# Optimization experiments

Measured on AMD Instinct MI355X. Metric: run time of the kernel, lower is better.

Reference implementation:

```python
import jax, jax.numpy as jnp
import numpy as np

EPS_BN = 1e-5
EPS_LN = 1e-5

def _bn(x, gamma, beta, ch_axis):
    # training-mode BatchNorm: batch stats over all axes except ch_axis (biased var)
    axes = tuple(i for i in range(x.ndim) if i != ch_axis)
    mean = x.mean(axes, keepdims=True)
    var = x.var(axes, keepdims=True)
    shp = [1] * x.ndim; shp[ch_axis] = -1
    return (x - mean) / jnp.sqrt(var + EPS_BN) * gamma.reshape(shp) + beta.reshape(shp)

def _ln(x, gamma, beta):
    mean = x.mean(-1, keepdims=True)
    var = x.var(-1, keepdims=True)
    return (x - mean) / jnp.sqrt(var + EPS_LN) * gamma + beta

def _spline(x, knots, cps):
    # x: (B,S); knots, cps: (K,). Single-pass bucketize + gather + lerp,
    # equivalent to the torch per-interval masked loop (boundary points take
    # the right interval's t=0 value, identical result).
    K = knots.shape[0]
    xn = (x - jnp.min(x)) / (jnp.max(x) - jnp.min(x) + 1e-6)
    idx = jnp.clip(jnp.searchsorted(knots, xn, side='right') - 1, 0, K - 2)
    k0, k1 = knots[idx], knots[idx + 1]
    t = (xn - k0) / (k1 - k0)
    val = (1.0 - t) * cps[idx] + t * cps[idx + 1]
    in_range = (xn >= knots[0]) & (xn <= knots[-1])
    return jnp.where(in_range, val, 0.0)

def _mha(x, in_w, in_b, out_w, out_b, H):
    # torch nn.MultiheadAttention with batch_first=False: dim0 is the sequence.
    L, N, D = x.shape
    hd = D // H
    qkv = x @ in_w.T + in_b                       # (L,N,3D)
    q, k, v = jnp.split(qkv, 3, axis=-1)
    q = q.reshape(L, N, H, hd) * (1.0 / np.sqrt(hd))
    k = k.reshape(L, N, H, hd)
    v = v.reshape(L, N, H, hd)
    scores = jnp.einsum('lnhd,mnhd->nhlm', q, k)  # (N,H,L,L)
    attn = jax.nn.softmax(scores, axis=-1)
    out = jnp.einsum('nhlm,mnhd->lnhd', attn, v).reshape(L, N, D)
    return out @ out_w.T + out_b

def setup_inputs() -> dict:
    B, S, D, F, K, H = 32, 1024, 512, 8, 32, 8
    key = jax.random.key(0)
    ks = jax.random.split(key, 12)
    s = 0.02
    inp = {
        'x': jax.random.normal(ks[0], (B, S, D), jnp.float32),
        'in_w': jax.random.normal(ks[1], (3 * D, D), jnp.float32) * s,
        'in_b': jnp.zeros((3 * D,), jnp.float32),
        'out_w': jax.random.normal(ks[2], (D, D), jnp.float32) * s,
        'out_b': jnp.zeros((D,), jnp.float32),
        'attn_g': jnp.ones((D,), jnp.float32),
        'attn_beta': jnp.zeros((D,), jnp.float32),
        'proj_w': jax.random.normal(ks[3], (F, D), jnp.float32) * s,
        'proj_b': jnp.zeros((F,), jnp.float32),
        'pn_g': jnp.ones((F,), jnp.float32),
        'pn_beta': jnp.zeros((F,), jnp.float32),
        'knots': jnp.tile(jnp.linspace(0.0, 1.0, K, dtype=jnp.float32)[None, :], (F, 1)),
        'cps': jax.random.normal(ks[4], (F, K), jnp.float32) / np.sqrt(K),
        'gate_w': jax.random.normal(ks[5], (2 * D, F), jnp.float32) * s,
        'gate_b': jnp.zeros((2 * D,), jnp.float32),
        'gbn_g': jnp.ones((S,), jnp.float32),   # BatchNorm1d(2*d_model) hits dim1 = seq (= 2*d_model)
        'gbn_beta': jnp.zeros((S,), jnp.float32),
        'ln_g': jnp.ones((D,), jnp.float32),
        'ln_beta': jnp.zeros((D,), jnp.float32),
        'outp_w': jax.random.normal(ks[6], (D, D), jnp.float32) * s,
        'outp_b': jnp.zeros((D,), jnp.float32),
        'on_g': jnp.ones((D,), jnp.float32),
        'on_beta': jnp.zeros((D,), jnp.float32),
    }
    return inp

def reference(x, in_w, in_b, out_w, out_b, attn_g, attn_beta, proj_w, proj_b,
              pn_g, pn_beta, knots, cps, gate_w, gate_b, gbn_g, gbn_beta,
              ln_g, ln_beta, outp_w, outp_b, on_g, on_beta):
    H = 8
    attn_out = _mha(x, in_w, in_b, out_w, out_b, H)          # (B,S,D)
    attn_out = _bn(attn_out, attn_g, attn_beta, 2)
    projected = x @ proj_w.T + proj_b                         # (B,S,F)
    projected = _bn(projected, pn_g, pn_beta, 2)
    transformed = jax.vmap(_spline, in_axes=(2, 0, 0), out_axes=2)(projected, knots, cps)  # (B,S,F)
    h = transformed @ gate_w.T + gate_b                       # (B,S,2D)
    h = _bn(h, gbn_g, gbn_beta, 1)                            # channel axis = seq (torch quirk)
    a, b = jnp.split(h, 2, axis=-1)
    glu = a * jax.nn.sigmoid(b)                               # (B,S,D)
    gated = _ln(glu, ln_g, ln_beta)
    out = gated @ outp_w.T + outp_b
    out = _bn(out, on_g, on_beta, 2)
    return x + attn_out + out
```

## Files before the change

### kernel.cpp

```cpp
#include <hip/hip_runtime.h>
#include <math.h>


#define SOFF_AMEAN 0
#define SOFF_ARSTD 512
#define SOFF_OMEAN 1024
#define SOFF_ORSTD 1536
#define SOFF_PMEAN 2048
#define SOFF_PRSTD 2056
#define SOFF_FMIN  2064
#define SOFF_FMAX  2072
#define SOFF_SMEAN 2080
#define SOFF_SRSTD 3104
#define SOFF_G1    4128
#define SOFF_GB    4136
#define SOFF_SGB   4144
#define SOFF_QGB   4145
#define SOFF_G2    4160
#define SOFF_PART  4224

typedef short bf16x8_t __attribute__((ext_vector_type(8)));
typedef float f32x4_t __attribute__((ext_vector_type(4)));
typedef unsigned short us8_t __attribute__((ext_vector_type(8)));

__device__ __forceinline__ unsigned short f2bf(float f) {
  unsigned u = __float_as_uint(f);
  u = (u + 0x7FFFu + ((u >> 16) & 1u)) >> 16;
  return (unsigned short)u;
}
__device__ __forceinline__ float b2f(unsigned short u) {
  return __uint_as_float(((unsigned)u) << 16);
}

#define BARR do { asm volatile("" ::: "memory"); __builtin_amdgcn_s_barrier(); asm volatile("" ::: "memory"); } while (0)

__global__ __launch_bounds__(256) void zero_kernel(float* __restrict__ p) {
  p[blockIdx.x * 256 + threadIdx.x] = 0.f;
}

__global__ __launch_bounds__(256) void cvt8_kernel(const float* __restrict__ src,
                                                   unsigned short* __restrict__ dst) {
  int i = blockIdx.x * 256 + threadIdx.x;
  float4 a = ((const float4*)src)[i * 2];
  float4 b = ((const float4*)src)[i * 2 + 1];
  us8_t o;
  o[0] = f2bf(a.x); o[1] = f2bf(a.y); o[2] = f2bf(a.z); o[3] = f2bf(a.w);
  o[4] = f2bf(b.x); o[5] = f2bf(b.y); o[6] = f2bf(b.z); o[7] = f2bf(b.w);
  *(us8_t*)(dst + (size_t)i * 8) = o;
}

template<int NT, bool OUT_BF16, bool STATS>
__global__ __launch_bounds__(512, 2) void gemm256_kernel(
    const unsigned short* __restrict__ A, const unsigned short* __restrict__ B,
    const float* __restrict__ bias, unsigned short* __restrict__ Cb,
    float* __restrict__ Cf, float* __restrict__ gstats, int N) {
  __shared__ unsigned short As[2][256 * 64];
  __shared__ unsigned short Bs[2][256 * 64];
  const int bi = blockIdx.x;
  const int xcd = bi & 7, jb = bi >> 3;
  const int m0 = (xcd * 16 + jb / NT) * 256;
  const int n0 = (jb % NT) * 256;
  const int t = threadIdx.x;
  const int w = t >> 6, lane = t & 63;
  const int wm = w >> 2, wn = w & 3;

  const int srow = lane >> 3;
  const int sgo = ((lane & 7) ^ srow) * 8;
  const unsigned short* gA = A + (size_t)(m0 + w * 32 + srow) * 512 + sgo;
  const unsigned short* gB = B + (size_t)(n0 + w * 32 + srow) * 512 + sgo;

  const int fr = lane & 15, g = lane >> 4;
  const int swz = fr & 7;

  f32x4_t acc[8][4];
#pragma unroll
  for (int i = 0; i < 8; ++i)
#pragma unroll
    for (int jj = 0; jj < 4; ++jj) acc[i][jj] = (f32x4_t){0.f, 0.f, 0.f, 0.f};

#define STAGE(SX, KO) do { \
  _Pragma("unroll") for (int jj = 0; jj < 4; ++jj) { \
    __builtin_amdgcn_global_load_lds( \
        (const __attribute__((address_space(1))) void*)(gA + (size_t)jj * 8 * 512 + (KO)), \
        (__attribute__((address_space(3))) void*)&As[SX][(w * 32 + jj * 8) * 64], 16, 0, 0); \
    __builtin_amdgcn_global_load_lds( \
        (const __attribute__((address_space(1))) void*)(gB + (size_t)jj * 8 * 512 + (KO)), \
        (__attribute__((address_space(3))) void*)&Bs[SX][(w * 32 + jj * 8) * 64], 16, 0, 0); \
  } \
} while (0)

#define RDA(MI0) do { \
  _Pragma("unroll") for (int m2 = 0; m2 < 2; ++m2) \
    _Pragma("unroll") for (int ks = 0; ks < 2; ++ks) \
      af[m2][ks] = *(const bf16x8_t*)&as[((wm * 128 + (MI0 + m2) * 16 + fr) * 64) + (((ks * 4 + g) ^ swz) * 8)]; \
} while (0)

#define QUAD(MI0) do { \
  __builtin_amdgcn_s_setprio(1); \
  _Pragma("unroll") for (int ks = 0; ks < 2; ++ks) \
    _Pragma("unroll") for (int m2 = 0; m2 < 2; ++m2) \
      _Pragma("unroll") for (int ni = 0; ni < 4; ++ni) \
        acc[MI0 + m2][ni] = __builtin_amdgcn_mfma_f32_16x16x32_bf16(af[m2][ks], bfr[ni][ks], acc[MI0 + m2][ni], 0, 0, 0); \
  __builtin_amdgcn_s_setprio(0); \
} while (0)

  STAGE(0, (size_t)0);
  asm volatile("s_waitcnt vmcnt(0)" ::: "memory");
  BARR;

#pragma unroll 2
  for (int kt = 0; kt < 8; ++kt) {
    const int sd = kt & 1;
    const unsigned short* as = &As[sd][0];
    const unsigned short* bs = &Bs[sd][0];
    bf16x8_t bfr[4][2], af[2][2];

#pragma unroll
    for (int ni = 0; ni < 4; ++ni)
#pragma unroll
      for (int ks = 0; ks < 2; ++ks)
        bfr[ni][ks] = *(const bf16x8_t*)&bs[((wn * 64 + ni * 16 + fr) * 64) + (((ks * 4 + g) ^ swz) * 8)];
    RDA(0);
    if (kt < 7) STAGE(sd ^ 1, (size_t)(kt + 1) * 64);
    BARR;
    QUAD(0);
    BARR;
    RDA(2);
    BARR;
    QUAD(2);
    BARR;
    RDA(4);
    BARR;
    QUAD(4);
    BARR;
    RDA(6);
    BARR;
    QUAD(6);
    if (kt < 7) asm volatile("s_waitcnt vmcnt(0)" ::: "memory");
    BARR;
  }

  const int cr = (lane >> 4) * 4, cc = lane & 15;
#pragma unroll
  for (int ni = 0; ni < 4; ++ni) {
    int col = n0 + wn * 64 + ni * 16 + cc;
    float bv = bias[col];
    float lsum = 0.f, lsq = 0.f;
#pragma unroll
    for (int mi = 0; mi < 8; ++mi) {
#pragma unroll
      for (int jj = 0; jj < 4; ++jj) {
        int row = m0 + wm * 128 + mi * 16 + cr + jj;
        float v = acc[mi][ni][jj] + bv;
        if (OUT_BF16) Cb[(size_t)row * N + col] = f2bf(v);
        else          Cf[(size_t)row * N + col] = v;
        if (STATS) { lsum += v; lsq += v * v; }
      }
    }
    if (STATS) {
      lsum += __shfl_xor(lsum, 16); lsum += __shfl_xor(lsum, 32);
      lsq  += __shfl_xor(lsq, 16);  lsq  += __shfl_xor(lsq, 32);
      if (lane < 16) {
        atomicAdd(&gstats[col], lsum);
        atomicAdd(&gstats[512 + col], lsq);
      }
    }
  }
#undef STAGE
#undef RDA
#undef QUAD
}

__global__ __launch_bounds__(512) void statsfin_kernel(const float* __restrict__ part,
                                                       float* __restrict__ stats, int off) {
  int t = threadIdx.x;
  float mean = part[t] / 32768.f;
  float var = part[512 + t] / 32768.f - mean * mean;
  stats[off + t] = mean;
  stats[off + 512 + t] = rsqrtf(var + 1e-5f);
}

__global__ __launch_bounds__(256) void attn2_kernel(const unsigned short* __restrict__ qkv,
                                                    unsigned short* __restrict__ ctxb) {
  const int n = blockIdx.x, h = blockIdx.y, t = threadIdx.x;
  __shared__ float qs[32 * 68], ks[32 * 68], vs[32 * 68], ss[32 * 33];
  const int l = t >> 3, j0 = (t & 7) * 8;
  size_t rowb = ((size_t)(l * 1024 + n)) * 1536 + h * 64 + j0;
  us8_t qv = *(const us8_t*)(qkv + rowb);
  us8_t kv = *(const us8_t*)(qkv + rowb + 512);
  us8_t vv = *(const us8_t*)(qkv + rowb + 1024);
#pragma unroll
  for (int j = 0; j < 8; ++j) {
    qs[l * 68 + j0 + j] = b2f(qv[j]) * 0.125f;
    ks[l * 68 + j0 + j] = b2f(kv[j]);
    vs[l * 68 + j0 + j] = b2f(vv[j]);
  }
  __syncthreads();
  for (int o = t; o < 1024; o += 256) {
    int ll = o >> 5, m = o & 31;
    const float4* q4 = (const float4*)&qs[ll * 68];
    const float4* k4 = (const float4*)&ks[m * 68];
    float s = 0.f;
#pragma unroll
    for (int dd = 0; dd < 16; ++dd) {
      float4 a = q4[dd], b = k4[dd];
      s += a.x * b.x + a.y * b.y + a.z * b.z + a.w * b.w;
    }
    ss[ll * 33 + m] = s;
  }
  __syncthreads();
  if (t < 32) {
    float mx = -3e38f;
    for (int m = 0; m < 32; ++m) mx = fmaxf(mx, ss[t * 33 + m]);
    float sum = 0.f;
    for (int m = 0; m < 32; ++m) { float e = __expf(ss[t * 33 + m] - mx); ss[t * 33 + m] = e; sum += e; }
    float inv = 1.f / sum;
    for (int m = 0; m < 32; ++m) ss[t * 33 + m] *= inv;
  }
  __syncthreads();
  float o[8] = {0.f, 0.f, 0.f, 0.f, 0.f, 0.f, 0.f, 0.f};
#pragma unroll 8
  for (int m = 0; m < 32; ++m) {
    float pm = ss[l * 33 + m];
    const float* vr = &vs[m * 68 + j0];
#pragma unroll
    for (int j = 0; j < 8; ++j) o[j] += pm * vr[j];
  }
  us8_t ov;
#pragma unroll
  for (int j = 0; j < 8; ++j) ov[j] = f2bf(o[j]);
  *(us8_t*)(ctxb + ((size_t)(l * 1024 + n)) * 512 + h * 64 + j0) = ov;
}

__global__ __launch_bounds__(256) void proj_kernel(const float* __restrict__ x,
    const float* __restrict__ pw, const float* __restrict__ pb, float* __restrict__ p) {
  int blk = blockIdx.x, t = threadIdx.x;
  int r0 = blk * 64;
  __shared__ float xsp[64 * 33];
  __shared__ float pwc[8 * 33];
  int l = t >> 2, fg = t & 3;
  float acc0 = 0.f, acc1 = 0.f;
  for (int k0 = 0; k0 < 512; k0 += 32) {
    __syncthreads();
    for (int i = t; i < 2048; i += 256) { int ll = i >> 5, kk = i & 31; xsp[ll * 33 + kk] = x[(size_t)(r0 + ll) * 512 + k0 + kk]; }
    { int ff = t >> 5, kk = t & 31; pwc[ff * 33 + kk] = pw[ff * 512 + k0 + kk]; }
    __syncthreads();
#pragma unroll 8
    for (int kk = 0; kk < 32; ++kk) {
      float xv = xsp[l * 33 + kk];
      acc0 += xv * pwc[(fg * 2) * 33 + kk];
      acc1 += xv * pwc[(fg * 2 + 1) * 33 + kk];
    }
  }
  float2 o; o.x = acc0 + pb[fg * 2]; o.y = acc1 + pb[fg * 2 + 1];
  *(float2*)&p[(r0 + l) * 8 + fg * 2] = o;
}

__global__ __launch_bounds__(256) void projstats_kernel(const float* __restrict__ p,
                                                        float* __restrict__ part) {
  int t = threadIdx.x, blk = blockIdx.x;
  int f = t & 7;
  float s = 0.f, s2 = 0.f;
  for (int r = blk * 32 + (t >> 3); r < 32768; r += 2048) { float v = p[r * 8 + f]; s += v; s2 += v * v; }
  __shared__ float red[256], red2[256];
  red[t] = s; red2[t] = s2; __syncthreads();
  for (int off = 128; off >= 8; off >>= 1) { if (t < off) { red[t] += red[t + off]; red2[t] += red2[t + off]; } __syncthreads(); }
  if (t < 8) { part[blk * 16 + t] = red[t]; part[blk * 16 + 8 + t] = red2[t]; }
}
__global__ void projfin_kernel(const float* __restrict__ part, float* __restrict__ stats) {
  int t = threadIdx.x;
  if (t < 8) {
    float s = 0.f, s2 = 0.f;
    for (int b = 0; b < 64; ++b) { s += part[b * 16 + t]; s2 += part[b * 16 + 8 + t]; }
    float mean = s / 32768.f;
    float var = s2 / 32768.f - mean * mean;
    stats[SOFF_PMEAN + t] = mean;
    stats[SOFF_PRSTD + t] = rsqrtf(var + 1e-5f);
  }
}

__global__ __launch_bounds__(256) void bnminmax_kernel(float* __restrict__ p,
    const float* __restrict__ stats, const float* __restrict__ png,
    const float* __restrict__ pnb, float* __restrict__ part) {
  int t = threadIdx.x, blk = blockIdx.x;
  int i0 = blk * 256 + t;
  int f = i0 & 7;
  float k1 = stats[SOFF_PRSTD + f] * png[f];
  float k0 = pnb[f] - stats[SOFF_PMEAN + f] * k1;
  float mn = 3e38f, mx = -3e38f;
  for (int i = i0; i < 262144; i += 16384) {
    float v = p[i] * k1 + k0;
    p[i] = v;
    mn = fminf(mn, v); mx = fmaxf(mx, v);
  }
  __shared__ float rmn[256], rmx[256];
  rmn[t] = mn; rmx[t] = mx; __syncthreads();
  for (int off = 128; off >= 8; off >>= 1) {
    if (t < off) { rmn[t] = fminf(rmn[t], rmn[t + off]); rmx[t] = fmaxf(rmx[t], rmx[t + off]); }
    __syncthreads();
  }
  if (t < 8) { part[blk * 16 + t] = rmn[t]; part[blk * 16 + 8 + t] = rmx[t]; }
}
__global__ void minmaxfin_kernel(const float* __restrict__ part, float* __restrict__ stats) {
  int t = threadIdx.x;
  if (t < 8) {
    float mn = 3e38f, mx = -3e38f;
    for (int b = 0; b < 64; ++b) { mn = fminf(mn, part[b * 16 + t]); mx = fmaxf(mx, part[b * 16 + 8 + t]); }
    stats[SOFF_FMIN + t] = mn;
    stats[SOFF_FMAX + t] = mx;
  }
}

__global__ __launch_bounds__(256) void spline_kernel(float* __restrict__ p,
    const float* __restrict__ knots, const float* __restrict__ cps,
    const float* __restrict__ stats) {
  __shared__ float ksh[8 * 33], csh[8 * 33];
  int t = threadIdx.x;
  { int f = t >> 5, j = t & 31; ksh[f * 33 + j] = knots[t]; csh[f * 33 + j] = cps[t]; }
  __syncthreads();
  int i = blockIdx.x * 256 + t;
  int f = i & 7;
  float xv = p[i];
  float mn = stats[SOFF_FMIN + f], mx = stats[SOFF_FMAX + f];
  float xn = (xv - mn) / (mx - mn + 1e-6f);
  const float* kn = &ksh[f * 33];
  const float* cp = &csh[f * 33];
  int pcnt = 0;
#pragma unroll
  for (int j = 0; j < 32; ++j) pcnt += (kn[j] <= xn) ? 1 : 0;
  int idx = pcnt - 1;
  idx = idx < 0 ? 0 : (idx > 30 ? 30 : idx);
  float k0v = kn[idx], k1v = kn[idx + 1];
  float tt = (xn - k0v) / (k1v - k0v);
  float val = (1.f - tt) * cp[idx] + tt * cp[idx + 1];
  bool inr = (xn >= kn[0]) && (xn <= kn[31]);
  p[i] = inr ? val : 0.f;
}

__global__ __launch_bounds__(256) void gateprep_kernel(const float* __restrict__ gw,
    const float* __restrict__ gb, float* __restrict__ stats) {
  int b = blockIdx.x, t = threadIdx.x;
  __shared__ float red[256];
  float s = 0.f;
  if (b < 64) {
    int f1 = b >> 3, f2 = b & 7;
    for (int j = t; j < 1024; j += 256) s += gw[j * 8 + f1] * gw[j * 8 + f2];
  } else if (b < 72) {
    int f = b - 64;
    for (int j = t; j < 1024; j += 256) s += gw[j * 8 + f];
  } else if (b < 80) {
    int f = b - 72;
    for (int j = t; j < 1024; j += 256) s += gb[j] * gw[j * 8 + f];
  } else if (b == 80) {
    for (int j = t; j < 1024; j += 256) s += gb[j];
  } else {
    for (int j = t; j < 1024; j += 256) s += gb[j] * gb[j];
  }
  red[t] = s; __syncthreads();
  for (int off = 128; off > 0; off >>= 1) { if (t < off) red[t] += red[t + off]; __syncthreads(); }
  if (t == 0) {
    float v = red[0];
    if (b < 64) stats[SOFF_G2 + b] = v;
    else if (b < 72) stats[SOFF_G1 + (b - 64)] = v;
    else if (b < 80) stats[SOFF_GB + (b - 72)] = v;
    else if (b == 80) stats[SOFF_SGB] = v;
    else stats[SOFF_QGB] = v;
  }
}

__global__ __launch_bounds__(256) void sstats_kernel(const float* __restrict__ tbuf,
                                                     float* __restrict__ stats) {
  int s = blockIdx.x, t = threadIdx.x;
  __shared__ float tv[256];
  __shared__ float red[256];
  __shared__ float T1[8];
  __shared__ float Ms[64];
  int b = t >> 3, f = t & 7;
  tv[t] = tbuf[(b * 1024 + s) * 8 + f];
  __syncthreads();
  red[t] = tv[t]; __syncthreads();
  for (int off = 128; off >= 8; off >>= 1) { if (t < off) red[t] += red[t + off]; __syncthreads(); }
  if (t < 8) T1[t] = red[t];
  if (t < 64) {
    int f1 = t >> 3, f2 = t & 7; float sM = 0.f;
    for (int bb = 0; bb < 32; ++bb) sM += tv[bb * 8 + f1] * tv[bb * 8 + f2];
    Ms[t] = sM;
  }
  __syncthreads();
  if (t == 0) {
    float sh = 0.f, s2 = 0.f;
    for (int ff = 0; ff < 8; ++ff) {
      sh += stats[SOFF_G1 + ff] * T1[ff];
      s2 += 2.f * stats[SOFF_GB + ff] * T1[ff];
    }
    sh += 32.f * stats[SOFF_SGB];
    for (int i = 0; i < 64; ++i) s2 += Ms[i] * stats[SOFF_G2 + i];
    s2 += 32.f * stats[SOFF_QGB];
    float mean = sh / 32768.f;
    float var = s2 / 32768.f - mean * mean;
    stats[SOFF_SMEAN + s] = mean;
    stats[SOFF_SRSTD + s] = rsqrtf(var + 1e-5f);
  }
}

__global__ __launch_bounds__(256) void gluln_kernel(const float* __restrict__ tbuf,
    const float* __restrict__ gw, const float* __restrict__ gb,
    const float* __restrict__ stats, const float* __restrict__ gbng,
    const float* __restrict__ gbnb, const float* __restrict__ lng,
    const float* __restrict__ lnb, unsigned short* __restrict__ gatedb) {
  const int t = threadIdx.x, wave = t >> 6, lane = t & 63;
  for (int rr = 0; rr < 4; ++rr) {
    const int r = blockIdx.x * 16 + wave * 4 + rr;
    const int s = r & 1023;
    float4 tA = *(const float4*)&tbuf[r * 8];
    float4 tB = *(const float4*)&tbuf[r * 8 + 4];
    float smean = stats[SOFF_SMEAN + s], srstd = stats[SOFF_SRSTD + s];
    float k1 = srstd * gbng[s];
    float k0 = gbnb[s] - smean * k1;
    float g[8];
    float sum = 0.f, sq = 0.f;
#pragma unroll
    for (int i = 0; i < 8; ++i) {
      int c = i * 64 + lane;
      float4 wa0 = *(const float4*)&gw[c * 8];
      float4 wa1 = *(const float4*)&gw[c * 8 + 4];
      float4 wb0 = *(const float4*)&gw[(c + 512) * 8];
      float4 wb1 = *(const float4*)&gw[(c + 512) * 8 + 4];
      float ha = tA.x * wa0.x + tA.y * wa0.y + tA.z * wa0.z + tA.w * wa0.w
               + tB.x * wa1.x + tB.y * wa1.y + tB.z * wa1.z + tB.w * wa1.w + gb[c];
      float hb = tA.x * wb0.x + tA.y * wb0.y + tA.z * wb0.z + tA.w * wb0.w
               + tB.x * wb1.x + tB.y * wb1.y + tB.z * wb1.z + tB.w * wb1.w + gb[c + 512];
      ha = ha * k1 + k0;
      hb = hb * k1 + k0;
      float gv = ha / (1.f + __expf(-hb));
      g[i] = gv; sum += gv; sq += gv * gv;
    }
#pragma unroll
    for (int m = 32; m >= 1; m >>= 1) { sum += __shfl_xor(sum, m); sq += __shfl_xor(sq, m); }
    float mean = sum * (1.f / 512.f);
    float rstd = rsqrtf(sq * (1.f / 512.f) - mean * mean + 1e-5f);
#pragma unroll
    for (int i = 0; i < 8; ++i) {
      int c = i * 64 + lane;
      gatedb[(size_t)r * 512 + c] = f2bf((g[i] - mean) * rstd * lng[c] + lnb[c]);
    }
  }
}

__global__ __launch_bounds__(256) void final_kernel(const float* __restrict__ x,
    const float* __restrict__ attn, const float* __restrict__ outl,
    const float* __restrict__ stats, const float* __restrict__ ag,
    const float* __restrict__ ab, const float* __restrict__ og,
    const float* __restrict__ ob, float* __restrict__ y) {
  int idx = blockIdx.x * 256 + threadIdx.x;
  int c4 = (idx & 127) * 4;
  float4 xv = ((const float4*)x)[idx];
  float4 av = ((const float4*)attn)[idx];
  float4 ov = ((const float4*)outl)[idx];
  float4 am = *(const float4*)&stats[SOFF_AMEAN + c4];
  float4 ar = *(const float4*)&stats[SOFF_ARSTD + c4];
  float4 om = *(const float4*)&stats[SOFF_OMEAN + c4];
  float4 orr = *(const float4*)&stats[SOFF_ORSTD + c4];
  float4 g1 = *(const float4*)&ag[c4];
  float4 b1 = *(const float4*)&ab[c4];
  float4 g2 = *(const float4*)&og[c4];
  float4 b2 = *(const float4*)&ob[c4];
  float4 o;
  o.x = xv.x + (av.x - am.x) * ar.x * g1.x + b1.x + (ov.x - om.x) * orr.x * g2.x + b2.x;
  o.y = xv.y + (av.y - am.y) * ar.y * g1.y + b1.y + (ov.y - om.y) * orr.y * g2.y + b2.y;
  o.z = xv.z + (av.z - am.z) * ar.z * g1.z + b1.z + (ov.z - om.z) * orr.z * g2.z + b2.z;
  o.w = xv.w + (av.w - am.w) * ar.w * g1.w + b1.w + (ov.w - om.w) * orr.w * g2.w + b2.w;
  ((float4*)y)[idx] = o;
}

extern "C" void kernel_launch(void* const* d_in, const int* in_sizes, int n_in,
                              void* d_out, int out_size, void* d_ws, size_t ws_size,
                              hipStream_t stream) {
  (void)in_sizes; (void)n_in; (void)out_size; (void)ws_size;
  const float* x        = (const float*)d_in[0];
  const float* in_w     = (const float*)d_in[1];
  const float* in_b     = (const float*)d_in[2];
  const float* out_w    = (const float*)d_in[3];
  const float* out_b    = (const float*)d_in[4];
  const float* attn_g   = (const float*)d_in[5];
  const float* attn_bt  = (const float*)d_in[6];
  const float* proj_w   = (const float*)d_in[7];
  const float* proj_b   = (const float*)d_in[8];
  const float* pn_g     = (const float*)d_in[9];
  const float* pn_bt    = (const float*)d_in[10];
  const float* knots    = (const float*)d_in[11];
  const float* cps      = (const float*)d_in[12];
  const float* gate_w   = (const float*)d_in[13];
  const float* gate_b   = (const float*)d_in[14];
  const float* gbn_g    = (const float*)d_in[15];
  const float* gbn_bt   = (const float*)d_in[16];
  const float* ln_g     = (const float*)d_in[17];
  const float* ln_bt    = (const float*)d_in[18];
  const float* outp_w   = (const float*)d_in[19];
  const float* outp_b   = (const float*)d_in[20];
  const float* on_g     = (const float*)d_in[21];
  const float* on_bt    = (const float*)d_in[22];

  float* out = (float*)d_out;
  unsigned short* xb      = (unsigned short*)d_ws;
  unsigned short* qkv_b   = xb + 16777216;
  unsigned short* ctx_b   = qkv_b + 50331648;
  unsigned short* wqkv_b  = ctx_b + 16777216;
  unsigned short* wout_b  = wqkv_b + 786432;
  unsigned short* woutp_b = wout_b + 262144;
  float* proj  = (float*)(woutp_b + 262144);
  float* stats = proj + 262144;
  float* part  = stats + SOFF_PART;
  float* partA  = part;
  float* partO  = part + 1024;
  float* partP  = part + 2048;
  float* partMM = part + 3072;
  float* attnf = (float*)qkv_b;
  unsigned short* gated_b = xb;

  zero_kernel<<<dim3(8), dim3(256), 0, stream>>>(part);
  cvt8_kernel<<<dim3(8192), dim3(256), 0, stream>>>(x, xb);
  cvt8_kernel<<<dim3(384), dim3(256), 0, stream>>>(in_w, wqkv_b);
  cvt8_kernel<<<dim3(128), dim3(256), 0, stream>>>(out_w, wout_b);
  cvt8_kernel<<<dim3(128), dim3(256), 0, stream>>>(outp_w, woutp_b);
  gemm256_kernel<6, true, false><<<dim3(768), dim3(512), 0, stream>>>(
      xb, wqkv_b, in_b, qkv_b, nullptr, nullptr, 1536);
  attn2_kernel<<<dim3(1024, 8), dim3(256), 0, stream>>>(qkv_b, ctx_b);
  gemm256_kernel<2, false, true><<<dim3(256), dim3(512), 0, stream>>>(
      ctx_b, wout_b, out_b, nullptr, attnf, partA, 512);
  statsfin_kernel<<<dim3(1), dim3(512), 0, stream>>>(partA, stats, SOFF_AMEAN);
  proj_kernel<<<dim3(512), dim3(256), 0, stream>>>(x, proj_w, proj_b, proj);
  projstats_kernel<<<dim3(64), dim3(256), 0, stream>>>(proj, partP);
  projfin_kernel<<<dim3(1), dim3(64), 0, stream>>>(partP, stats);
  bnminmax_kernel<<<dim3(64), dim3(256), 0, stream>>>(proj, stats, pn_g, pn_bt, partMM);
  minmaxfin_kernel<<<dim3(1), dim3(64), 0, stream>>>(partMM, stats);
  spline_kernel<<<dim3(1024), dim3(256), 0, stream>>>(proj, knots, cps, stats);
  gateprep_kernel<<<dim3(88), dim3(256), 0, stream>>>(gate_w, gate_b, stats);
  sstats_kernel<<<dim3(1024), dim3(256), 0, stream>>>(proj, stats);
  gluln_kernel<<<dim3(2048), dim3(256), 0, stream>>>(proj, gate_w, gate_b, stats,
                                                     gbn_g, gbn_bt, ln_g, ln_bt, gated_b);
  gemm256_kernel<2, false, true><<<dim3(256), dim3(512), 0, stream>>>(
      gated_b, woutp_b, outp_b, nullptr, out, partO, 512);
  statsfin_kernel<<<dim3(1), dim3(512), 0, stream>>>(partO, stats, SOFF_OMEAN);
  final_kernel<<<dim3(16384), dim3(256), 0, stream>>>(x, attnf, out, stats,
                                                      attn_g, attn_bt, on_g, on_bt, out);
}
```

Before: 534.0 us.

## Restructure GEMM main loop into 4-stage K=32 LDS pipeline with single barrier

The 256x256 bf16 GEMM now streams K in 32-wide slices through a 4-deep LDS ring (prefetch distance 3) instead of 64-wide double buffering. Each iteration loads all A/B fragments and issues 32 MFMAs with one barrier, instead of four read/compute phases separated by many barriers. The epilogue is also reordered to iterate rows outer and columns inner, with per-column partial stats. The aim is to hide global load latency and cut barrier overhead. In exchange it keeps more fragment registers live and uses a new LDS swizzle for the narrower rows.

```diff
diff --git a/kernel.cpp b/kernel.cpp
--- a/kernel.cpp
+++ b/kernel.cpp
@@ -54,8 +54,8 @@
     const unsigned short* __restrict__ A, const unsigned short* __restrict__ B,
     const float* __restrict__ bias, unsigned short* __restrict__ Cb,
     float* __restrict__ Cf, float* __restrict__ gstats, int N) {
-  __shared__ unsigned short As[2][256 * 64];
-  __shared__ unsigned short Bs[2][256 * 64];
+  __shared__ unsigned short As[4][256 * 32];
+  __shared__ unsigned short Bs[4][256 * 32];
   const int bi = blockIdx.x;
   const int xcd = bi & 7, jb = bi >> 3;
   const int m0 = (xcd * 16 + jb / NT) * 256;
@@ -64,13 +64,13 @@
   const int w = t >> 6, lane = t & 63;
   const int wm = w >> 2, wn = w & 3;
 
-  const int srow = lane >> 3;
-  const int sgo = ((lane & 7) ^ srow) * 8;
-  const unsigned short* gA = A + (size_t)(m0 + w * 32 + srow) * 512 + sgo;
-  const unsigned short* gB = B + (size_t)(n0 + w * 32 + srow) * 512 + sgo;
+  const unsigned short* gA = A + (size_t)(m0 + w * 16 + (lane >> 2)) * 512
+                               + (((lane & 3) ^ ((lane >> 3) & 3)) * 8);
+  const unsigned short* gB = B + (size_t)(n0 + w * 16 + (lane >> 2)) * 512
+                               + (((lane & 3) ^ ((lane >> 3) & 3)) * 8);
 
   const int fr = lane & 15, g = lane >> 4;
-  const int swz = fr & 7;
+  const int kf = (fr >> 1) & 3;
 
   f32x4_t acc[8][4];
 #pragma unroll
@@ -78,97 +78,88 @@
 #pragma unroll
     for (int jj = 0; jj < 4; ++jj) acc[i][jj] = (f32x4_t){0.f, 0.f, 0.f, 0.f};
 
-#define STAGE(SX, KO) do { \
-  _Pragma("unroll") for (int jj = 0; jj < 4; ++jj) { \
+#define STAGE(KT) do { \
     __builtin_amdgcn_global_load_lds( \
-        (const __attribute__((address_space(1))) void*)(gA + (size_t)jj * 8 * 512 + (KO)), \
-        (__attribute__((address_space(3))) void*)&As[SX][(w * 32 + jj * 8) * 64], 16, 0, 0); \
+        (const __attribute__((address_space(1))) void*)(gA + (KT) * 32), \
+        (__attribute__((address_space(3))) void*)&As[(KT) & 3][(w * 16) * 32], 16, 0, 0); \
     __builtin_amdgcn_global_load_lds( \
-        (const __attribute__((address_space(1))) void*)(gB + (size_t)jj * 8 * 512 + (KO)), \
-        (__attribute__((address_space(3))) void*)&Bs[SX][(w * 32 + jj * 8) * 64], 16, 0, 0); \
-  } \
-} while (0)
-
-#define RDA(MI0) do { \
-  _Pragma("unroll") for (int m2 = 0; m2 < 2; ++m2) \
-    _Pragma("unroll") for (int ks = 0; ks < 2; ++ks) \
-      af[m2][ks] = *(const bf16x8_t*)&as[((wm * 128 + (MI0 + m2) * 16 + fr) * 64) + (((ks * 4 + g) ^ swz) * 8)]; \
-} while (0)
-
-#define QUAD(MI0) do { \
-  __builtin_amdgcn_s_setprio(1); \
-  _Pragma("unroll") for (int ks = 0; ks < 2; ++ks) \
-    _Pragma("unroll") for (int m2 = 0; m2 < 2; ++m2) \
-      _Pragma("unroll") for (int ni = 0; ni < 4; ++ni) \
-        acc[MI0 + m2][ni] = __builtin_amdgcn_mfma_f32_16x16x32_bf16(af[m2][ks], bfr[ni][ks], acc[MI0 + m2][ni], 0, 0, 0); \
-  __builtin_amdgcn_s_setprio(0); \
-} while (0)
-
-  STAGE(0, (size_t)0);
-  asm volatile("s_waitcnt vmcnt(0)" ::: "memory");
+        (const __attribute__((address_space(1))) void*)(gA + (KT) * 32 + 128 * 512), \
+        (__attribute__((address_space(3))) void*)&As[(KT) & 3][(128 + w * 16) * 32], 16, 0, 0); \
+    __builtin_amdgcn_global_load_lds( \
+        (const __attribute__((address_space(1))) void*)(gB + (KT) * 32), \
+        (__attribute__((address_space(3))) void*)&Bs[(KT) & 3][(w * 16) * 32], 16, 0, 0); \
+    __builtin_amdgcn_global_load_lds( \
+        (const __attribute__((address_space(1))) void*)(gB + (KT) * 32 + 128 * 512), \
+        (__attribute__((address_space(3))) void*)&Bs[(KT) & 3][(128 + w * 16) * 32], 16, 0, 0); \
+  } while (0)
+
+  STAGE(0); STAGE(1); STAGE(2);
+  asm volatile("s_waitcnt vmcnt(8)" ::: "memory");
   BARR;
 
-#pragma unroll 2
-  for (int kt = 0; kt < 8; ++kt) {
-    const int sd = kt & 1;
-    const unsigned short* as = &As[sd][0];
-    const unsigned short* bs = &Bs[sd][0];
-    bf16x8_t bfr[4][2], af[2][2];
-
+#pragma unroll
+  for (int kt = 0; kt < 16; ++kt) {
+    if (kt < 13) STAGE(kt + 3);
+    const unsigned short* asb = &As[kt & 3][0];
+    const unsigned short* bsb = &Bs[kt & 3][0];
+    bf16x8_t af[8], bf[4];
 #pragma unroll
     for (int ni = 0; ni < 4; ++ni)
-#pragma unroll
-      for (int ks = 0; ks < 2; ++ks)
-        bfr[ni][ks] = *(const bf16x8_t*)&bs[((wn * 64 + ni * 16 + fr) * 64) + (((ks * 4 + g) ^ swz) * 8)];
-    RDA(0);
-    if (kt < 7) STAGE(sd ^ 1, (size_t)(kt + 1) * 64);
-    BARR;
-    QUAD(0);
-    BARR;
-    RDA(2);
-    BARR;
-    QUAD(2);
-    BARR;
-    RDA(4);
-    BARR;
-    QUAD(4);
-    BARR;
-    RDA(6);
-    BARR;
-    QUAD(6);
-    if (kt < 7) asm volatile("s_waitcnt vmcnt(0)" ::: "memory");
-    BARR;
-  }
+      bf[ni] = *(const bf16x8_t*)&bsb[(wn * 64 + ni * 16 + fr) * 32 + ((g ^ kf) * 8)];
+#pragma unroll
+    for (int mi = 0; mi < 8; ++mi)
+      af[mi] = *(const bf16x8_t*)&asb[(wm * 128 + mi * 16 + fr) * 32 + ((g ^ kf) * 8)];
+    __builtin_amdgcn_s_setprio(1);
+#pragma unroll
+    for (int mi = 0; mi < 8; ++mi)
+#pragma unroll
+      for (int ni = 0; ni < 4; ++ni)
+        acc[mi][ni] = __builtin_amdgcn_mfma_f32_16x16x32_bf16(af[mi], bf[ni], acc[mi][ni], 0, 0, 0);
+    __builtin_amdgcn_s_setprio(0);
+    if (kt < 15) {
+      if (kt <= 12)      asm volatile("s_waitcnt vmcnt(8)" ::: "memory");
+      else if (kt == 13) asm volatile("s_waitcnt vmcnt(4)" ::: "memory");
+      else               asm volatile("s_waitcnt vmcnt(0)" ::: "memory");
+      BARR;
+    }
+  }
+#undef STAGE
 
   const int cr = (lane >> 4) * 4, cc = lane & 15;
+  float bv[4], lsum[4], lsq[4];
 #pragma unroll
   for (int ni = 0; ni < 4; ++ni) {
-    int col = n0 + wn * 64 + ni * 16 + cc;
-    float bv = bias[col];
-    float lsum = 0.f, lsq = 0.f;
-#pragma unroll
-    for (int mi = 0; mi < 8; ++mi) {
-#pragma unroll
-      for (int jj = 0; jj < 4; ++jj) {
-        int row = m0 + wm * 128 + mi * 16 + cr + jj;
-        float v = acc[mi][ni][jj] + bv;
-        if (OUT_BF16) Cb[(size_t)row * N + col] = f2bf(v);
-        else          Cf[(size_t)row * N + col] = v;
-        if (STATS) { lsum += v; lsq += v * v; }
+    bv[ni] = bias[n0 + wn * 64 + ni * 16 + cc];
+    lsum[ni] = 0.f; lsq[ni] = 0.f;
+  }
+#pragma unroll
+  for (int mi = 0; mi < 8; ++mi) {
+#pragma unroll
+    for (int jj = 0; jj < 4; ++jj) {
+      const size_t row = (size_t)(m0 + wm * 128 + mi * 16 + cr + jj);
+#pragma unroll
+      for (int ni = 0; ni < 4; ++ni) {
+        int col = n0 + wn * 64 + ni * 16 + cc;
+        float v = acc[mi][ni][jj] + bv[ni];
+        if (OUT_BF16) Cb[row * N + col] = f2bf(v);
+        else          Cf[row * N + col] = v;
+        if (STATS) { lsum[ni] += v; lsq[ni] += v * v; }
       }
     }
-    if (STATS) {
-      lsum += __shfl_xor(lsum, 16); lsum += __shfl_xor(lsum, 32);
-      lsq  += __shfl_xor(lsq, 16);  lsq  += __shfl_xor(lsq, 32);
+  }
+  if (STATS) {
+#pragma unroll
+    for (int ni = 0; ni < 4; ++ni) {
+      float s = lsum[ni], q = lsq[ni];
+      s += __shfl_xor(s, 16); s += __shfl_xor(s, 32);
+      q += __shfl_xor(q, 16); q += __shfl_xor(q, 32);
       if (lane < 16) {
-        atomicAdd(&gstats[col], lsum);
-        atomicAdd(&gstats[512 + col], lsq);
+        int col = n0 + wn * 64 + ni * 16 + lane;
+        atomicAdd(&gstats[col], s);
+        atomicAdd(&gstats[512 + col], q);
       }
     }
   }
-#undef STAGE
-#undef RDA
-#undef QUAD
 }
 
 __global__ __launch_bounds__(512) void statsfin_kernel(const float* __restrict__ part,
```

Result: faster. 522.5 us (-2.2%).
